# Kernel tuning notes

Measured on AMD Instinct MI355X. Metric: run time of the kernel, lower is better.

The kernel has to match this reference:

```python
import jax, jax.numpy as jnp
import numpy as np

N = 4096      # atoms
K = 5         # atoms gathered per cell (top_k in put_atoms_in_cells)
M = 8         # neighbors kept per atom
NBR = 26      # neighbor cells per cell (9+9+8)

def _grid():
    # get_cells: box [-10,10) step 1 Angstrom -> 20^3 = 8000 cells
    g = jnp.arange(-10.0, 10.0, 1.0)
    X = jnp.stack(jnp.meshgrid(g, g, g))       # (3,20,20,20), tf.meshgrid default 'xy'
    return jnp.transpose(X).reshape(-1, 3)      # (8000,3)

def _sqdist(a, b):
    # ||a_i - b_j||^2 via expansion; avoids (A,B,3) intermediate
    return (jnp.sum(a * a, 1)[:, None] + jnp.sum(b * b, 1)[None, :] - 2.0 * (a @ b.T))

def _neighbor_list(coords):
    cells = _grid()                              # (n_cells, 3)
    # put_atoms_in_cells: tf.nn.top_k(norm, k) -> k LARGEST norms (faithful to source)
    d_ca = _sqdist(cells, coords)                # (n_cells, N)
    _, atoms_in_cells = jax.lax.top_k(d_ca, K)   # (n_cells, K)
    # get_cells_for_atoms: top_k(-norm, 1) -> closest cell per atom
    d_ac = _sqdist(coords, cells)                # (N, n_cells)
    cells_for_atoms = jnp.argmin(d_ac, axis=1)   # (N,)
    # compute_neighbor_cells: top_k(norm, 26) (faithful to source)
    d_cc = _sqdist(cells, cells)                 # (n_cells, n_cells)
    _, nbr_cells = jax.lax.top_k(d_cc, NBR)      # (n_cells, 26)
    nbr_cells_atom = nbr_cells[cells_for_atoms]  # (N, 26)
    nbr_inds = atoms_in_cells[nbr_cells_atom]    # (N, 26, K)
    nbr_coords = coords[nbr_inds]                # (N, 26, K, 3)
    dists = jnp.sum((coords[:, None, None, :] - nbr_coords) ** 2, axis=-1)
    dists = dists.reshape(N, NBR * K)            # (N, 130)
    _, locs = jax.lax.top_k(dists, M)            # top_k(dists, M) as in source
    flat = nbr_inds.reshape(N, NBR * K)
    return jnp.take_along_axis(flat, locs, axis=1)   # (N, M) atom indices

def _energy(coords, vdw, weights, nrot, nbr):
    # d_ij = r_ij - R_i - R_j
    diff = coords[:, None, :] - coords[nbr]      # (N, M, 3)
    r = jnp.sqrt(jnp.sum(diff * diff, axis=-1) + 1e-12)
    d = r - vdw[:, None] - vdw[nbr]
    g1 = jnp.exp(-(d / 0.5) ** 2)
    g2 = jnp.exp(-((d - 3.0) / 2.0) ** 2)
    rep = jnp.where(d < 0.0, d * d, 0.0)
    hyd = jnp.where(d < 0.5, 1.0, jnp.where(d < 1.5, 1.5 - d, 0.0))
    hb = jnp.where(d < -0.7, 1.0, jnp.where(d < 0.0, -d / 0.7, 0.0))
    hval = (weights[0] * g1 + weights[1] * g2 + weights[2] * rep
            + weights[3] * hyd + weights[4] * hb)
    f = jnp.where(d < 8.0, hval, 0.0)            # cutoff at 8 Angstrom
    c = jnp.sum(f)
    return c / (1.0 + weights[5] * nrot[0])      # g(c, Nrot)

def setup_inputs() -> dict:
    key = jax.random.key(0)
    k1, k2, k3 = jax.random.split(key, 3)
    coords = jax.random.uniform(k1, (N, 3), jnp.float32, -10.0, 10.0)
    vdw = jax.random.uniform(k2, (N,), jnp.float32, 1.0, 2.0)
    weights = 0.3 * jax.random.normal(k3, (6,), jnp.float32)
    nrot = 8.0 * jnp.ones((1,), jnp.float32)
    return {"coords": coords, "vdw": vdw, "weights": weights, "nrot": nrot}

def reference(coords, vdw, weights, nrot):
    nbr = _neighbor_list(coords)
    return _energy(coords, vdw, weights, nrot, nbr)
```

## Files before the change

kernel.cpp:

```cpp
#include <hip/hip_runtime.h>
#include <stdint.h>

#define NATOMS 4096
#define NCELLS 8000
#define KTOP 5
#define MNBR 8
#define NBRC 26
#define HBINS 184
#define LSTMAX 512

__device__ __forceinline__ unsigned long long umax64(unsigned long long a, unsigned long long b) {
    return a > b ? a : b;
}
__device__ __forceinline__ unsigned long long umin64(unsigned long long a, unsigned long long b) {
    return a < b ? a : b;
}

__device__ __forceinline__ void cell_coords_i(int m, int& x, int& y, int& z) {
    int a = m / 400;
    int r = m - a * 400;
    int b = r / 20;
    int c = r - b * 20;
    x = b - 10; y = c - 10; z = a - 10;
}

__global__ __launch_bounds__(256) void k1_cells_nbr(const float* __restrict__ coords,
                                                    int* __restrict__ cellsForAtoms,
                                                    float4* __restrict__ c4,
                                                    int* __restrict__ nbrTable,
                                                    int* __restrict__ neededFlag) {
    const int atom = blockIdx.x;
    const int t = threadIdx.x;
    const int lane = t & 63;

    __shared__ int sCi;
    __shared__ uint32_t h[HBINS];
    __shared__ int lst[LSTMAX];
    __shared__ int sV, cnt;

    if (t < HBINS) h[t] = 0;
    if (t == 0) cnt = 0;

    if (t < 64) {
        float ax = coords[atom * 3], ay = coords[atom * 3 + 1], az = coords[atom * 3 + 2];
        float sa = __fadd_rn(__fadd_rn(__fmul_rn(ax, ax), __fmul_rn(ay, ay)), __fmul_rn(az, az));

        int fx = (int)floorf(ax), fy = (int)floorf(ay), fz = (int)floorf(az);
        int vx = min(9, max(-10, fx - 1 + (lane & 3)));
        int vy = min(9, max(-10, fy - 1 + ((lane >> 2) & 3)));
        int vz = min(9, max(-10, fz - 1 + (lane >> 4)));
        int m = (vz + 10) * 400 + (vx + 10) * 20 + (vy + 10);

        float cx = (float)vx, cy = (float)vy, cz = (float)vz;
        float scell = (float)(vx * vx + vy * vy + vz * vz);
        float dot = __fadd_rn(__fadd_rn(__fmul_rn(ax, cx), __fmul_rn(ay, cy)), __fmul_rn(az, cz));
        float val = __fsub_rn(__fadd_rn(sa, scell), __fmul_rn(2.0f, dot));
        unsigned long long key = ((unsigned long long)__float_as_uint(val) << 32) | (unsigned int)m;

        for (int off = 32; off > 0; off >>= 1)
            key = umin64(key, (unsigned long long)__shfl_xor((long long)key, off));
        if (lane == 0) {
            int c = (int)(key & 0xFFFFFFFFull);
            cellsForAtoms[atom] = c;
            c4[atom] = make_float4(ax, ay, az, sa);
            sCi = c;
        }
    }
    __syncthreads();

    const int ci = sCi;
    int xi, yi, zi;
    cell_coords_i(ci, xi, yi, zi);
    const int Lx = max(xi + 10, 9 - xi);
    const int Ly = max(yi + 10, 9 - yi);
    const int Lz = max(zi + 10, 9 - zi);
    const int lo = (Lx - 2) * (Lx - 2) + (Ly - 2) * (Ly - 2) + (Lz - 2) * (Lz - 2)
                 + 2 * min(Lx, min(Ly, Lz)) - 3;
    const int A0 = zi + 10;

#pragma unroll
    for (int col = 0; col < 2; ++col) {
        int p = t + 256 * col;
        if (p < 400) {
            int bb = p / 20, cc = p - bb * 20;
            int dxv = xi - (bb - 10), dyv = yi - (cc - 10);
            int Dbc = dxv * dxv + dyv * dyv;
            int a = 0;
            for (; a < 20; ++a) {
                int dz = A0 - a;
                int d = Dbc + dz * dz;
                if (d < lo) break;
                atomicAdd(&h[d - lo], 1u);
            }
            if (a < 20) {
                for (int a2 = 19; a2 >= a; --a2) {
                    int dz = A0 - a2;
                    int d = Dbc + dz * dz;
                    if (d < lo) break;
                    atomicAdd(&h[d - lo], 1u);
                }
            }
        }
    }
    __syncthreads();

    if (t < 64) {
        int c4b[4];
        int cnt4 = 0;
#pragma unroll
        for (int k = 0; k < 4; ++k) {
            int b = (HBINS - 1) - (t * 4 + k);
            c4b[k] = (b >= 0) ? (int)h[b] : 0;
            cnt4 += c4b[k];
        }
        int incl = cnt4;
        for (int off = 1; off < 64; off <<= 1) {
            int v = __shfl_up(incl, off);
            if (lane >= off) incl += v;
        }
        int P = incl - cnt4;
        if (P < NBRC && incl >= NBRC) {
            int run = P;
#pragma unroll
            for (int k = 0; k < 4; ++k) {
                run += c4b[k];
                if (run >= NBRC) { sV = lo + (HBINS - 1) - (t * 4 + k); break; }
            }
        }
    }
    __syncthreads();
    const int V = sV;

#pragma unroll
    for (int col = 0; col < 2; ++col) {
        int p = t + 256 * col;
        if (p < 400) {
            int bb = p / 20, cc = p - bb * 20;
            int dxv = xi - (bb - 10), dyv = yi - (cc - 10);
            int Dbc = dxv * dxv + dyv * dyv;
            int a = 0;
            for (; a < 20; ++a) {
                int dz = A0 - a;
                int d = Dbc + dz * dz;
                if (d < V) break;
                int q = atomicAdd(&cnt, 1);
                if (q < LSTMAX) lst[q] = (d << 13) | (8191 - (a * 400 + p));
            }
            if (a < 20) {
                for (int a2 = 19; a2 >= a; --a2) {
                    int dz = A0 - a2;
                    int d = Dbc + dz * dz;
                    if (d < V) break;
                    int q = atomicAdd(&cnt, 1);
                    if (q < LSTMAX) lst[q] = (d << 13) | (8191 - (a2 * 400 + p));
                }
            }
        }
    }
    __syncthreads();

    int n = min(cnt, LSTMAX);
    for (int idx = t; idx < n; idx += 256) {
        int key = lst[idx];
        int rank = 0;
        for (int m = 0; m < n; ++m) rank += (lst[m] > key) ? 1 : 0;
        if (rank < NBRC) {
            int j = 8191 - (key & 8191);
            nbrTable[ci * NBRC + rank] = j;
            neededFlag[j] = 1;
        }
    }
}

__global__ __launch_bounds__(256) void k2_atoms(const float4* __restrict__ c4,
                                                const int* __restrict__ neededFlag,
                                                int* __restrict__ atomsInCells) {
    const int i = blockIdx.x;
    if (neededFlag[i] != 1) return;
    __shared__ unsigned long long wl[4 * KTOP];
    const int t = threadIdx.x;
    const int lane = t & 63, wv = t >> 6;

    int xi_, yi_, zi_;
    cell_coords_i(i, xi_, yi_, zi_);
    const float cx = (float)xi_, cy = (float)yi_, cz = (float)zi_;
    const float scell = (float)(xi_ * xi_ + yi_ * yi_ + zi_ * zi_);

    unsigned long long keys[16];
#pragma unroll
    for (int s = 0; s < 16; ++s) {
        int j = t + 256 * s;
        float4 v = c4[j];
        float dot = __fadd_rn(__fadd_rn(__fmul_rn(cx, v.x), __fmul_rn(cy, v.y)),
                              __fmul_rn(cz, v.z));
        float val = __fsub_rn(__fadd_rn(scell, v.w), __fmul_rn(2.0f, dot));
        keys[s] = ((unsigned long long)__float_as_uint(val) << 32) | (unsigned int)(4095 - j);
    }

    for (int r = 0; r < KTOP; ++r) {
        unsigned long long best = 0ull;
#pragma unroll
        for (int s = 0; s < 16; ++s) best = umax64(best, keys[s]);
        for (int off = 32; off > 0; off >>= 1)
            best = umax64(best, (unsigned long long)__shfl_xor((long long)best, off));
        if (lane == 0) wl[wv * KTOP + r] = best;
#pragma unroll
        for (int s = 0; s < 16; ++s) if (keys[s] == best) keys[s] = 0ull;
    }
    __syncthreads();

    if (t < 4 * KTOP) {
        unsigned long long key = wl[t];
        int rank = 0;
        for (int m = 0; m < 4 * KTOP; ++m) rank += (wl[m] > key) ? 1 : 0;
        if (rank < KTOP) atomsInCells[i * KTOP + rank] = 4095 - (int)(key & 0xFFFFFFFFull);
    }
}

__global__ __launch_bounds__(256) void k3_energy(const float4* __restrict__ c4,
                                                 const float* __restrict__ vdw,
                                                 const float* __restrict__ weights,
                                                 const int* __restrict__ nbrTable,
                                                 const int* __restrict__ atomsInCells,
                                                 const int* __restrict__ cellsForAtoms,
                                                 float* __restrict__ partials) {
    const int wid = threadIdx.x >> 6;
    const int lane = threadIdx.x & 63;
    const int i = blockIdx.x * 4 + wid;

    const float4 vi4 = c4[i];
    const float xi = vi4.x, yi = vi4.y, zi = vi4.z;
    const int ci = cellsForAtoms[i];

    int cand[3];
    unsigned long long keys[3];
#pragma unroll
    for (int s = 0; s < 3; ++s) {
        int p = lane + 64 * s;
        cand[s] = -1;
        keys[s] = 0ull;
        if (p < NBRC * KTOP) {
            int cellSlot = p / KTOP;
            int atomSlot = p - cellSlot * KTOP;
            int nc = nbrTable[ci * NBRC + cellSlot];
            int j = atomsInCells[nc * KTOP + atomSlot];
            cand[s] = j;
            float4 vj = c4[j];
            float dx = __fsub_rn(xi, vj.x);
            float dy = __fsub_rn(yi, vj.y);
            float dz = __fsub_rn(zi, vj.z);
            float dist = __fadd_rn(__fadd_rn(__fmul_rn(dx, dx), __fmul_rn(dy, dy)), __fmul_rn(dz, dz));
            keys[s] = ((unsigned long long)__float_as_uint(dist) << 8) | (unsigned int)(255 - p);
        }
    }

    const float w0 = weights[0], w1 = weights[1], w2 = weights[2];
    const float w3 = weights[3], w4 = weights[4];
    const float vi = vdw[i];

    float esum = 0.0f;
    for (int r = 0; r < MNBR; ++r) {
        unsigned long long best = umax64(umax64(keys[0], keys[1]), keys[2]);
        for (int off = 32; off > 0; off >>= 1)
            best = umax64(best, (unsigned long long)__shfl_xor((long long)best, off));

        int p = 255 - (int)(best & 0xFFull);
        int slot = p >> 6;
        int owner = p & 63;
        int jsel = (slot == 0) ? cand[0] : (slot == 1) ? cand[1] : cand[2];
        int j = __shfl(jsel, owner);
        float dist = __uint_as_float((unsigned int)(best >> 8));

#pragma unroll
        for (int s = 0; s < 3; ++s) if (keys[s] == best) keys[s] = 0ull;

        float rr = __fsqrt_rn(__fadd_rn(dist, 1e-12f));
        float d = __fsub_rn(__fsub_rn(rr, vi), vdw[j]);
        float t1 = __fdiv_rn(d, 0.5f);
        float g1 = expf(-__fmul_rn(t1, t1));
        float t2 = __fdiv_rn(__fsub_rn(d, 3.0f), 2.0f);
        float g2 = expf(-__fmul_rn(t2, t2));
        float rep = (d < 0.0f) ? __fmul_rn(d, d) : 0.0f;
        float hyd = (d < 0.5f) ? 1.0f : ((d < 1.5f) ? __fsub_rn(1.5f, d) : 0.0f);
        float hb = (d < -0.7f) ? 1.0f : ((d < 0.0f) ? __fdiv_rn(-d, 0.7f) : 0.0f);
        float hval = __fadd_rn(__fadd_rn(__fadd_rn(__fadd_rn(
                         __fmul_rn(w0, g1), __fmul_rn(w1, g2)),
                         __fmul_rn(w2, rep)), __fmul_rn(w3, hyd)), __fmul_rn(w4, hb));
        float f = (d < 8.0f) ? hval : 0.0f;
        esum = __fadd_rn(esum, f);
    }
    if (lane == 0) partials[i] = esum;
}

__global__ __launch_bounds__(256) void k4_reduce(const float* __restrict__ partials,
                                                 const float* __restrict__ weights,
                                                 const float* __restrict__ nrot,
                                                 float* __restrict__ out) {
    __shared__ float red[256];
    const int t = threadIdx.x;
    float s = 0.0f;
    for (int k = 0; k < NATOMS / 256; ++k) s = __fadd_rn(s, partials[t + 256 * k]);
    red[t] = s;
    __syncthreads();
    for (int off = 128; off > 0; off >>= 1) {
        if (t < off) red[t] = __fadd_rn(red[t], red[t + off]);
        __syncthreads();
    }
    if (t == 0) out[0] = __fdiv_rn(red[0], __fadd_rn(1.0f, __fmul_rn(weights[5], nrot[0])));
}

extern "C" void kernel_launch(void* const* d_in, const int* in_sizes, int n_in,
                              void* d_out, int out_size, void* d_ws, size_t ws_size,
                              hipStream_t stream) {
    const float* coords  = (const float*)d_in[0];
    const float* vdw     = (const float*)d_in[1];
    const float* weights = (const float*)d_in[2];
    const float* nrot    = (const float*)d_in[3];
    float* out = (float*)d_out;

    int* nbrTable      = (int*)d_ws;
    int* atomsInCells  = nbrTable + NCELLS * NBRC;
    int* cellsForAtoms = atomsInCells + NCELLS * KTOP;
    int* neededFlag    = cellsForAtoms + NATOMS;
    float* partials    = (float*)(neededFlag + NCELLS);
    float4* c4         = (float4*)(partials + NATOMS);

    k1_cells_nbr<<<NATOMS, 256, 0, stream>>>(coords, cellsForAtoms, c4,
                                             nbrTable, neededFlag);
    k2_atoms<<<NCELLS, 256, 0, stream>>>(c4, neededFlag, atomsInCells);
    k3_energy<<<NATOMS / 4, 256, 0, stream>>>(c4, vdw, weights, nbrTable,
                                              atomsInCells, cellsForAtoms, partials);
    k4_reduce<<<1, 256, 0, stream>>>(partials, weights, nrot, out);
}
```

Before: 39.36 us.

## Compute per-cell top-K with one wavefront per cell using running top-5 list

The atoms-in-cell top-K kernel now assigns one 64-lane wavefront per cell instead of a whole 256-thread block. Each lane keeps a sorted running top-5 in registers while streaming over the atoms, and five wave-wide max reductions then finalise the result without shared memory or __syncthreads. This cuts block count and the cross-wave merge, but each wave now does 64 serial iterations with divergent insertion branches instead of 16.

```diff
diff --git a/kernel.cpp b/kernel.cpp
--- a/kernel.cpp
+++ b/kernel.cpp
@@ -175,45 +175,42 @@
 __global__ __launch_bounds__(256) void k2_atoms(const float4* __restrict__ c4,
                                                 const int* __restrict__ neededFlag,
                                                 int* __restrict__ atomsInCells) {
-    const int i = blockIdx.x;
+    const int wv = threadIdx.x >> 6;
+    const int lane = threadIdx.x & 63;
+    const int i = blockIdx.x * 4 + wv;
     if (neededFlag[i] != 1) return;
-    __shared__ unsigned long long wl[4 * KTOP];
-    const int t = threadIdx.x;
-    const int lane = t & 63, wv = t >> 6;
 
     int xi_, yi_, zi_;
     cell_coords_i(i, xi_, yi_, zi_);
     const float cx = (float)xi_, cy = (float)yi_, cz = (float)zi_;
     const float scell = (float)(xi_ * xi_ + yi_ * yi_ + zi_ * zi_);
 
-    unsigned long long keys[16];
-#pragma unroll
-    for (int s = 0; s < 16; ++s) {
-        int j = t + 256 * s;
+    unsigned long long s0 = 0, s1 = 0, s2 = 0, s3 = 0, s4 = 0;
+    for (int it = 0; it < NATOMS / 64; ++it) {
+        int j = lane + 64 * it;
         float4 v = c4[j];
         float dot = __fadd_rn(__fadd_rn(__fmul_rn(cx, v.x), __fmul_rn(cy, v.y)),
                               __fmul_rn(cz, v.z));
         float val = __fsub_rn(__fadd_rn(scell, v.w), __fmul_rn(2.0f, dot));
-        keys[s] = ((unsigned long long)__float_as_uint(val) << 32) | (unsigned int)(4095 - j);
-    }
-
+        unsigned long long key =
+            ((unsigned long long)__float_as_uint(val) << 32) | (unsigned int)(4095 - j);
+        if (key > s4) {
+            if (key > s0)      { s4 = s3; s3 = s2; s2 = s1; s1 = s0; s0 = key; }
+            else if (key > s1) { s4 = s3; s3 = s2; s2 = s1; s1 = key; }
+            else if (key > s2) { s4 = s3; s3 = s2; s2 = key; }
+            else if (key > s3) { s4 = s3; s3 = key; }
+            else               { s4 = key; }
+        }
+    }
+
+#pragma unroll
     for (int r = 0; r < KTOP; ++r) {
-        unsigned long long best = 0ull;
-#pragma unroll
-        for (int s = 0; s < 16; ++s) best = umax64(best, keys[s]);
+        unsigned long long best = s0;
         for (int off = 32; off > 0; off >>= 1)
             best = umax64(best, (unsigned long long)__shfl_xor((long long)best, off));
-        if (lane == 0) wl[wv * KTOP + r] = best;
-#pragma unroll
-        for (int s = 0; s < 16; ++s) if (keys[s] == best) keys[s] = 0ull;
-    }
-    __syncthreads();
-
-    if (t < 4 * KTOP) {
-        unsigned long long key = wl[t];
-        int rank = 0;
-        for (int m = 0; m < 4 * KTOP; ++m) rank += (wl[m] > key) ? 1 : 0;
-        if (rank < KTOP) atomsInCells[i * KTOP + rank] = 4095 - (int)(key & 0xFFFFFFFFull);
+        if (s0 == best) { s0 = s1; s1 = s2; s2 = s3; s3 = s4; s4 = 0; }
+        if (lane == 0)
+            atomsInCells[i * KTOP + r] = 4095 - (int)(best & 0xFFFFFFFFull);
     }
 }
 
@@ -327,7 +324,7 @@
 
     k1_cells_nbr<<<NATOMS, 256, 0, stream>>>(coords, cellsForAtoms, c4,
                                              nbrTable, neededFlag);
-    k2_atoms<<<NCELLS, 256, 0, stream>>>(c4, neededFlag, atomsInCells);
+    k2_atoms<<<NCELLS / 4, 256, 0, stream>>>(c4, neededFlag, atomsInCells);
     k3_energy<<<NATOMS / 4, 256, 0, stream>>>(c4, vdw, weights, nbrTable,
                                               atomsInCells, cellsForAtoms, partials);
     k4_reduce<<<1, 256, 0, stream>>>(partials, weights, nrot, out);
```

After: 57.38 us. +45.8%, slower.
